# Kernel optimization log

Hardware: AMD Instinct MI355X
Metric: run time of the kernel (lower is better)

Reference implementation:

```python
import jax, jax.numpy as jnp
import numpy as np
from jax import lax

# Galaxy Zoo 2 question -> answer index ranges (start, end), keyed 1..11
Q_A = {1: (0, 3), 2: (3, 5), 3: (5, 7), 4: (7, 9), 5: (9, 13), 6: (13, 15),
       7: (15, 18), 8: (18, 25), 9: (25, 28), 10: (28, 31), 11: (31, 37)}
# Dependency map: answers whose probability multiplies the whole segment; [-1] = none
DEP = {1: [-1], 2: [1], 3: [4], 4: [4], 5: [4], 6: [-1],
       7: [0], 8: [13], 9: [3], 10: [7], 11: [7]}
BN_EPS = 1e-5


def _conv(x, w, b):
    y = lax.conv_general_dilated(x, w, (1, 1), 'VALID',
                                 dimension_numbers=('NCHW', 'OIHW', 'NCHW'))
    return y + b[None, :, None, None]


def _bn(x, s, b, m, v):  # eval-mode batchnorm with running stats
    inv = lax.rsqrt(v + BN_EPS)
    return (x - m[None, :, None, None]) * (s * inv)[None, :, None, None] + b[None, :, None, None]


def _pool(x):
    return lax.reduce_window(x, -jnp.inf, lax.max, (1, 1, 2, 2), (1, 1, 2, 2), 'VALID')


def _normalize(x):
    # Faithful to the in-place sequential torch loop: the segment sum is
    # recomputed after every element update, so earlier (already divided)
    # elements participate in later denominators. Fixed 37 steps, batched.
    for i in range(1, 12):
        s, e = Q_A[i]
        for j in range(s, e):
            seg_sum = jnp.sum(x[:, s:e], axis=1)
            x = x.at[:, j].set(x[:, j] / (seg_sum + 1e-12))
    return x


def _multiply_prob(x):
    # m = each[v] is read once before the inner j-loop, so a single
    # broadcast multiply over the segment is exactly equivalent.
    for i in range(1, 12):
        s, e = Q_A[i]
        vals = DEP[i]
        if vals[0] != -1:
            for v in vals:
                m = x[:, v:v + 1]  # [B,1], read before segment update
                x = x.at[:, s:e].multiply(m)
    return x


def _forward(x,
             conv1_w, conv1_b, bn1_s, bn1_b, bn1_m, bn1_v,
             conv2_w, conv2_b, bn2_s, bn2_b, bn2_m, bn2_v,
             conv3_w, conv3_b, bn3_s, bn3_b, bn3_m, bn3_v,
             conv4_w, conv4_b, bn4_s, bn4_b, bn4_m, bn4_v,
             fc1_w, fc1_b, fc2_w, fc2_b, fc3_w, fc3_b):
    # dropout layers are identity in eval mode
    h = _bn(jax.nn.relu(_conv(x, conv1_w, conv1_b)), bn1_s, bn1_b, bn1_m, bn1_v)
    h = _pool(_bn(jax.nn.relu(_conv(h, conv2_w, conv2_b)), bn2_s, bn2_b, bn2_m, bn2_v))
    h = _pool(_bn(jax.nn.relu(_conv(h, conv3_w, conv3_b)), bn3_s, bn3_b, bn3_m, bn3_v))
    h = _pool(_bn(jax.nn.relu(_conv(h, conv4_w, conv4_b)), bn4_s, bn4_b, bn4_m, bn4_v))
    h = h.reshape(-1, 3200)  # [B, 128*5*5]
    h = jax.nn.relu(h @ fc1_w.T + fc1_b)
    h = jax.nn.relu(h @ fc2_w.T + fc2_b)
    p = jax.nn.sigmoid(h @ fc3_w.T + fc3_b)  # [B, 37]
    return _multiply_prob(_normalize(p))


def setup_inputs() -> dict:
    key = jax.random.key(0)
    ks = iter(jax.random.split(key, 64))

    def n(shape, scale=0.05):
        return jax.random.normal(next(ks), shape, jnp.float32) * scale

    inp = {'x': jax.random.normal(next(ks), (1024, 3, 60, 60), jnp.float32)}
    convs = [(16, 3, 5), (32, 16, 5), (64, 32, 3), (128, 64, 3)]
    for ci, (o, i, kz) in enumerate(convs, 1):
        inp[f'conv{ci}_w'] = n((o, i, kz, kz))
        inp[f'conv{ci}_b'] = n((o,))
        inp[f'bn{ci}_s'] = 1.0 + n((o,))
        inp[f'bn{ci}_b'] = n((o,))
        inp[f'bn{ci}_m'] = n((o,))
        inp[f'bn{ci}_v'] = jax.random.uniform(next(ks), (o,), jnp.float32, 0.5, 1.5)
    inp['fc1_w'] = n((1024, 3200))
    inp['fc1_b'] = n((1024,))
    inp['fc2_w'] = n((512, 1024))
    inp['fc2_b'] = n((512,))
    inp['fc3_w'] = n((37, 512))
    inp['fc3_b'] = n((37,))
    return inp


def reference(x,
              conv1_w, conv1_b, bn1_s, bn1_b, bn1_m, bn1_v,
              conv2_w, conv2_b, bn2_s, bn2_b, bn2_m, bn2_v,
              conv3_w, conv3_b, bn3_s, bn3_b, bn3_m, bn3_v,
              conv4_w, conv4_b, bn4_s, bn4_b, bn4_m, bn4_v,
              fc1_w, fc1_b, fc2_w, fc2_b, fc3_w, fc3_b):
    return _forward(x,
                    conv1_w, conv1_b, bn1_s, bn1_b, bn1_m, bn1_v,
                    conv2_w, conv2_b, bn2_s, bn2_b, bn2_m, bn2_v,
                    conv3_w, conv3_b, bn3_s, bn3_b, bn3_m, bn3_v,
                    conv4_w, conv4_b, bn4_s, bn4_b, bn4_m, bn4_v,
                    fc1_w, fc1_b, fc2_w, fc2_b, fc3_w, fc3_b)
```

## Files before the change

kernel.cpp:

```cpp
#include <hip/hip_runtime.h>
#include <hip/hip_bf16.h>
#include <math.h>

constexpr int BATCH = 1024;
typedef unsigned short u16;
typedef unsigned long long u64;
typedef __attribute__((ext_vector_type(8))) short bf16x8;
typedef __attribute__((ext_vector_type(4))) float f32x4;
typedef __attribute__((ext_vector_type(16))) float f32x16;

__device__ __forceinline__ u16 f2bf(float f) {
    union { __hip_bfloat16 b; u16 s; } u; u.b = __float2bfloat16(f); return u.s;
}
__device__ __forceinline__ f32x4 mfma16(bf16x8 a, bf16x8 b, f32x4 c) {
    return __builtin_amdgcn_mfma_f32_16x16x32_bf16(a, b, c, 0, 0, 0);
}
__device__ __forceinline__ f32x16 mfma32(bf16x8 a, bf16x8 b, f32x16 c) {
    return __builtin_amdgcn_mfma_f32_32x32x16_bf16(a, b, c, 0, 0, 0);
}

__global__ __launch_bounds__(256)
void prep_all(const float* __restrict__ x,  const float* __restrict__ c1w,
              const float* __restrict__ c2w, const float* __restrict__ c3w,
              const float* __restrict__ c4w, const float* __restrict__ f1w,
              const float* __restrict__ f2w,
              u16* __restrict__ Xp,  u16* __restrict__ W1t, u16* __restrict__ W2t,
              u16* __restrict__ W3t, u16* __restrict__ W4t,
              u16* __restrict__ W1b, u16* __restrict__ W2b)
{
    int id = blockIdx.x * 256 + threadIdx.x;
    constexpr int NX   = 1024 * 3600;
    constexpr int NW1B = 819200;
    constexpr int NW2B = 131072;
    if (id < NX) {
        int img = id / 3600, p = id - img * 3600;
        const float* s = x + (size_t)img * 10800 + p;
        u16 pk[4] = { f2bf(s[0]), f2bf(s[3600]), f2bf(s[7200]), 0 };
        *(u64*)(Xp + (size_t)id * 4) = *(u64*)pk;
        return;
    }
    id -= NX;
    if (id < NW1B) {
        float4 v = ((const float4*)f1w)[id];
        u16 p[4] = { f2bf(v.x), f2bf(v.y), f2bf(v.z), f2bf(v.w) };
        *(u64*)(W1b + (size_t)id * 4) = *(u64*)p;
        return;
    }
    id -= NW1B;
    if (id < NW2B) {
        float4 v = ((const float4*)f2w)[id];
        u16 p[4] = { f2bf(v.x), f2bf(v.y), f2bf(v.z), f2bf(v.w) };
        *(u64*)(W2b + (size_t)id * 4) = *(u64*)p;
        return;
    }
    id -= NW2B;
    if (id < 2048) {
        int oc = id >> 7, k = id & 127, tap = k >> 2, ic = k & 3;
        W1t[id] = (ic < 3 && tap < 25) ? f2bf(c1w[oc * 75 + ic * 25 + tap]) : (u16)0;
        return;
    }
    id -= 2048;
    if (id < 12800) {
        int oc = id / 400, k = id - oc * 400;
        W2t[id] = f2bf(c2w[oc * 400 + (k & 15) * 25 + (k >> 4)]);
        return;
    }
    id -= 12800;
    if (id < 19456) {
        int oc = id / 304, k = id - oc * 304;
        W3t[id] = (k < 288) ? f2bf(c3w[oc * 288 + (k & 31) * 9 + (k >> 5)]) : (u16)0;
        return;
    }
    id -= 19456;
    if (id < 74752) {
        int oc = id / 584, k = id - oc * 584;
        W4t[id] = (k < 576) ? f2bf(c4w[oc * 576 + (k & 63) * 9 + (k >> 6)]) : (u16)0;
    }
}

__global__ __launch_bounds__(512, 4)
void conv12_fused(const u16* __restrict__ Xp,
                  const u16* __restrict__ W1t, const u16* __restrict__ W2t,
                  const float* __restrict__ c1b,
                  const float* __restrict__ b1s, const float* __restrict__ b1b,
                  const float* __restrict__ b1m, const float* __restrict__ b1v,
                  const float* __restrict__ c2b,
                  const float* __restrict__ b2s, const float* __restrict__ b2b,
                  const float* __restrict__ b2m, const float* __restrict__ b2v,
                  u16* __restrict__ out)
{
    __shared__ __align__(16) unsigned char S[54976];
    constexpr int U = 28800;
    float* s_bn1 = (float*)(S + 54400);
    float* s_bn2 = (float*)(S + 54592);

    const int tid = threadIdx.x;
    int bid = blockIdx.x;
    const int qx = bid & 1, qy = (bid >> 1) & 1, img = bid >> 2;

    const u64* XpI = (const u64*)Xp + (size_t)img * 3600 + (qy * 26) * 60 + qx * 26;
    for (int i = tid; i < 578; i += 512) {
        int row = i / 17, c2 = i - row * 17;
        *(bf16x8*)(S + U + (row * 34 + c2 * 2) * 8) =
            *(const bf16x8*)(XpI + row * 60 + c2 * 2);
    }
    for (int i = tid; i < 256; i += 512)
        *(bf16x8*)(S + U + 9248 + i * 16) = *(const bf16x8*)(W1t + i * 8);
    if (tid < 16) {
        float sc = b1s[tid] * rsqrtf(b1v[tid] + 1e-5f);
        s_bn1[tid] = c1b[tid]; s_bn1[16 + tid] = sc; s_bn1[32 + tid] = b1b[tid] - b1m[tid] * sc;
    } else if (tid >= 32 && tid < 64) {
        int t = tid - 32;
        float sc = b2s[t] * rsqrtf(b2v[t] + 1e-5f);
        s_bn2[t] = c2b[t]; s_bn2[32 + t] = sc; s_bn2[64 + t] = b2b[t] - b2m[t] * sc;
    }
    __syncthreads();

    const int wv = tid >> 6, lr = tid & 15, lg = (tid >> 4) & 3;
    const int o32 = tid & 31, hi = (tid >> 5) & 1;

    {
        int toff[4][2];
        #pragma unroll
        for (int ks = 0; ks < 4; ++ks)
            #pragma unroll
            for (int h = 0; h < 2; ++h) {
                int t = ks * 8 + lg * 2 + h; if (t > 24) t = 24;
                int ky = t / 5;
                toff[ks][h] = (ky * 34 + (t - ky * 5)) * 8;
            }
        bf16x8 wb[4];
        #pragma unroll
        for (int ks = 0; ks < 4; ++ks)
            wb[ks] = *(const bf16x8*)(S + U + 9248 + lr * 256 + ks * 64 + lg * 16);
        float4 bnB = *(const float4*)(s_bn1 + lg * 4);
        float4 bnS = *(const float4*)(s_bn1 + 16 + lg * 4);
        float4 bnH = *(const float4*)(s_bn1 + 32 + lg * 4);
        #pragma unroll
        for (int mi = 0; mi < 8; ++mi) {
            int t = wv + mi * 8;
            if (t < 57) {
                int pos = t * 16 + lr;
                int pc = pos > 899 ? 899 : pos;
                int py = pc / 30;
                int pb = (py * 34 + (pc - py * 30)) * 8;
                f32x4 a = {0.f, 0.f, 0.f, 0.f};
                #pragma unroll
                for (int ks = 0; ks < 4; ++ks) {
                    union { u64 v[2]; bf16x8 f; } xf;
                    xf.v[0] = *(const u64*)(S + U + pb + toff[ks][0]);
                    xf.v[1] = *(const u64*)(S + U + pb + toff[ks][1]);
                    a = mfma16(wb[ks], xf.f, a);
                }
                if (pos < 900) {
                    u16 q[4];
                    q[0] = f2bf(fmaxf(a[0] + bnB.x, 0.f) * bnS.x + bnH.x);
                    q[1] = f2bf(fmaxf(a[1] + bnB.y, 0.f) * bnS.y + bnH.y);
                    q[2] = f2bf(fmaxf(a[2] + bnB.z, 0.f) * bnS.z + bnH.z);
                    q[3] = f2bf(fmaxf(a[3] + bnB.w, 0.f) * bnS.w + bnH.w);
                    *(u64*)(S + pos * 32 + lg * 8) = *(u64*)q;
                }
            }
        }
    }
    __syncthreads();

    for (int i = tid; i < 1600; i += 512)
        *(bf16x8*)(S + U + i * 16) = *(const bf16x8*)(W2t + i * 8);
    __syncthreads();

    f32x16 acc[3];
    #pragma unroll
    for (int mi = 0; mi < 3; ++mi)
        #pragma unroll
        for (int j = 0; j < 16; ++j) acc[mi][j] = 0.f;
    int pbase[3];
    #pragma unroll
    for (int mi = 0; mi < 3; ++mi) {
        int tt = wv + mi * 8; if (tt > 21) tt = 21;
        int row = tt * 32 + o32;
        int q = row >> 2; if (q > 168) q = 168;
        int Q = row & 3;
        int y2 = 2 * (q / 13) + (Q >> 1);
        int x2 = 2 * (q - (q / 13) * 13) + (Q & 1);
        pbase[mi] = (y2 * 30 + x2) * 32 + hi * 16;
    }
    const unsigned char* wrow = S + U + o32 * 800 + hi * 16;
    #pragma unroll
    for (int ks = 0; ks < 25; ++ks) {
        bf16x8 b = *(const bf16x8*)(wrow + ks * 32);
        const int dp = ((ks / 5) * 30 + (ks % 5)) * 32;
        #pragma unroll
        for (int mi = 0; mi < 3; ++mi) {
            bf16x8 a = *(const bf16x8*)(S + pbase[mi] + dp);
            acc[mi] = mfma32(a, b, acc[mi]);
        }
    }
    u16* outI = out + (size_t)img * 676 * 32;
    float bnb = s_bn2[o32], bns = s_bn2[32 + o32], bnh = s_bn2[64 + o32];
    #pragma unroll
    for (int mi = 0; mi < 3; ++mi) {
        int tt = wv + mi * 8;
        if (tt < 22) {
            #pragma unroll
            for (int rg = 0; rg < 4; ++rg) {
                int quad = tt * 8 + 2 * rg + hi;
                if (quad < 169) {
                    float m = -3.4e38f;
                    #pragma unroll
                    for (int r = 0; r < 4; ++r)
                        m = fmaxf(m, fmaxf(acc[mi][rg * 4 + r] + bnb, 0.f) * bns + bnh);
                    int py = quad / 13, px = quad - (quad / 13) * 13;
                    int gpos = (qy * 13 + py) * 26 + qx * 13 + px;
                    outI[gpos * 32 + o32] = f2bf(m);
                }
            }
        }
    }
}

__global__ __launch_bounds__(576, 2)
void conv3_mfma(const u16* __restrict__ in, const u16* __restrict__ W3t,
                const float* __restrict__ cbias,
                const float* __restrict__ bns, const float* __restrict__ bnb,
                const float* __restrict__ bnm, const float* __restrict__ bnv,
                u16* __restrict__ out)
{
    __shared__ __align__(16) unsigned char S[63104];
    float* s_bn = (float*)(S + 62720);

    const int tid = threadIdx.x;
    const int ocg = blockIdx.x & 1;
    const int img = blockIdx.x >> 1;

    const u16* inI = in + (size_t)img * 676 * 32;
    for (int g = tid; g < 2704; g += 576) {
        int pa = g * 16;
        int off = pa ^ ((pa >> 2) & 0x20);
        *(bf16x8*)(S + off) = *(const bf16x8*)(inI + g * 8);
    }
    const u16* wsrc = W3t + ocg * 32 * 304;
    for (int i = tid; i < 1216; i += 576)
        *(bf16x8*)(S + 43264 + i * 16) = *(const bf16x8*)(wsrc + i * 8);
    if (tid < 32) {
        int oc = ocg * 32 + tid;
        float sc = bns[oc] * rsqrtf(bnv[oc] + 1e-5f);
        s_bn[tid] = cbias[oc]; s_bn[32 + tid] = sc; s_bn[64 + tid] = bnb[oc] - bnm[oc] * sc;
    }
    __syncthreads();

    const int wv = tid >> 6;
    const int o32 = tid & 31, hi = (tid >> 5) & 1;
    f32x16 acc[2];
    #pragma unroll
    for (int mi = 0; mi < 2; ++mi)
        #pragma unroll
        for (int j = 0; j < 16; ++j) acc[mi][j] = 0.f;
    int pbase[2];
    #pragma unroll
    for (int mi = 0; mi < 2; ++mi) {
        int tt = wv * 2 + mi;
        int row = tt * 32 + o32;
        int q = row >> 2, Q = row & 3;
        int y2 = 2 * (q / 12) + (Q >> 1);
        int x2 = 2 * (q - (q / 12) * 12) + (Q & 1);
        pbase[mi] = (y2 * 26 + x2) * 64 + hi * 16;
    }
    const unsigned char* wrow = S + 43264 + o32 * 608 + hi * 16;
    #pragma unroll
    for (int s = 0; s < 18; ++s) {
        bf16x8 b = *(const bf16x8*)(wrow + s * 32);
        const int cell = s >> 1;
        const int dp = ((cell / 3) * 26 + (cell % 3)) * 64 + (s & 1) * 32;
        #pragma unroll
        for (int mi = 0; mi < 2; ++mi) {
            int pa = pbase[mi] + dp;
            bf16x8 a = *(const bf16x8*)(S + (pa ^ ((pa >> 2) & 0x20)));
            acc[mi] = mfma32(a, b, acc[mi]);
        }
    }
    u16* outI = out + (size_t)img * 144 * 64 + ocg * 32;
    float bnbv = s_bn[o32], bnsv = s_bn[32 + o32], bnhv = s_bn[64 + o32];
    #pragma unroll
    for (int mi = 0; mi < 2; ++mi) {
        int tt = wv * 2 + mi;
        #pragma unroll
        for (int rg = 0; rg < 4; ++rg) {
            int quad = tt * 8 + 2 * rg + hi;
            float m = -3.4e38f;
            #pragma unroll
            for (int r = 0; r < 4; ++r)
                m = fmaxf(m, fmaxf(acc[mi][rg * 4 + r] + bnbv, 0.f) * bnsv + bnhv);
            outI[quad * 64 + o32] = f2bf(m);
        }
    }
}

__global__ __launch_bounds__(256)
void conv4_mfma(const u16* __restrict__ in, const u16* __restrict__ W4t,
                const float* __restrict__ cbias,
                const float* __restrict__ bns, const float* __restrict__ bnb,
                const float* __restrict__ bnm, const float* __restrict__ bnv,
                u16* __restrict__ out)
{
    __shared__ __align__(16) unsigned char S[56192];
    float* s_bn = (float*)(S + 55808);

    const int tid = threadIdx.x;
    const int ocg = blockIdx.x & 3;
    const int img = blockIdx.x >> 2;

    const u16* inI = in + (size_t)img * 144 * 64;
    for (int g = tid; g < 144 * 8; g += 256) {
        int pos = g >> 3, part = g & 7;
        int off = (pos * 128 + part * 16) ^ ((pos & 7) << 4);
        *(bf16x8*)(S + off) = *(const bf16x8*)(inI + g * 8);
    }
    const u16* wsrc = W4t + ocg * 32 * 584;
    for (int i = tid; i < 2336; i += 256)
        *(bf16x8*)(S + 18432 + i * 16) = *(const bf16x8*)(wsrc + i * 8);
    if (tid < 32) {
        int oc = ocg * 32 + tid;
        float sc = bns[oc] * rsqrtf(bnv[oc] + 1e-5f);
        s_bn[tid] = cbias[oc]; s_bn[32 + tid] = sc; s_bn[64 + tid] = bnb[oc] - bnm[oc] * sc;
    }
    __syncthreads();

    const int w = tid >> 6, lr = tid & 15, lg = (tid >> 4) & 3;
    f32x4 acc[2][2];
    {
        f32x4 z = {0.f, 0.f, 0.f, 0.f};
        acc[0][0] = z; acc[0][1] = z; acc[1][0] = z; acc[1][1] = z;
    }
    int pb7[2];
    #pragma unroll
    for (int mi = 0; mi < 2; ++mi) {
        int aq = (w + mi * 4) * 4 + (lr >> 2);
        if (aq > 24) aq = 24;
        int y2 = 2 * (aq / 5) + ((lr >> 1) & 1);
        int x2 = 2 * (aq % 5) + (lr & 1);
        pb7[mi] = ((y2 * 12 + x2) << 7) + lg * 16;
    }
    #pragma unroll
    for (int ks = 0; ks < 18; ++ks) {
        bf16x8 b0 = *(const bf16x8*)(S + 18432 + lr * 1168 + ks * 64 + lg * 16);
        bf16x8 b1 = *(const bf16x8*)(S + 18432 + (16 + lr) * 1168 + ks * 64 + lg * 16);
        const int cell = ks >> 1;
        const int dp7 = (((cell / 3) * 12 + (cell % 3)) << 7) + (ks & 1) * 64;
        #pragma unroll
        for (int mi = 0; mi < 2; ++mi) {
            int pa = pb7[mi] + dp7;
            int off = pa ^ ((pa >> 3) & 0x70);
            bf16x8 a = *(const bf16x8*)(S + off);
            acc[mi][0] = mfma16(a, b0, acc[mi][0]);
            acc[mi][1] = mfma16(a, b1, acc[mi][1]);
        }
    }
    u16* outI = out + (size_t)img * 3200;
    float bc0 = s_bn[lr],      sc0 = s_bn[32 + lr], sh0 = s_bn[64 + lr];
    float bc1 = s_bn[16 + lr], sc1 = s_bn[48 + lr], sh1 = s_bn[80 + lr];
    #pragma unroll
    for (int mi = 0; mi < 2; ++mi) {
        int quad = (w + mi * 4) * 4 + lg;
        if (quad < 25) {
            float m0 = -3.4e38f, m1 = -3.4e38f;
            #pragma unroll
            for (int r2 = 0; r2 < 4; ++r2) {
                m0 = fmaxf(m0, fmaxf(acc[mi][0][r2] + bc0, 0.f) * sc0 + sh0);
                m1 = fmaxf(m1, fmaxf(acc[mi][1][r2] + bc1, 0.f) * sc1 + sh1);
            }
            outI[(ocg * 32 + lr) * 25 + quad]      = f2bf(m0);
            outI[(ocg * 32 + 16 + lr) * 25 + quad] = f2bf(m1);
        }
    }
}

template<bool OUTF32>
__global__ __launch_bounds__(256)
void fc_gemm_bf(const u16* __restrict__ A, const u16* __restrict__ Wb,
                const float* __restrict__ bias, void* __restrict__ outv,
                int M, int N, int K)
{
    __shared__ __align__(16) unsigned char S[34816];
    const int tid = threadIdx.x;
    const int n0 = blockIdx.x * 64, m0 = blockIdx.y * 64;
    const int w = tid >> 6, lr = tid & 15, lg = (tid >> 4) & 3;
    const int r = tid >> 2, c = tid & 3;

    f32x4 acc[4];
    { f32x4 z = {0.f,0.f,0.f,0.f}; acc[0]=z; acc[1]=z; acc[2]=z; acc[3]=z; }

    const u16* Ab = A  + (size_t)(m0 + r) * K + c * 8;
    const u16* Bb = Wb + (size_t)(n0 + r) * K + c * 8;
    unsigned char* sAw = S + r * 272 + c * 16;
    unsigned char* sBw = S + 17408 + r * 272 + c * 16;

    for (int k0 = 0; k0 < K; k0 += 128) {
        #pragma unroll
        for (int q = 0; q < 4; ++q) {
            *(bf16x8*)(sAw + q * 64) = *(const bf16x8*)(Ab + k0 + q * 32);
            *(bf16x8*)(sBw + q * 64) = *(const bf16x8*)(Bb + k0 + q * 32);
        }
        __syncthreads();
        #pragma unroll
        for (int k32 = 0; k32 < 4; ++k32) {
            bf16x8 a = *(const bf16x8*)(S + (w * 16 + lr) * 272 + k32 * 64 + lg * 16);
            #pragma unroll
            for (int nt = 0; nt < 4; ++nt) {
                bf16x8 b = *(const bf16x8*)(S + 17408 + (nt * 16 + lr) * 272 + k32 * 64 + lg * 16);
                acc[nt] = mfma16(a, b, acc[nt]);
            }
        }
        __syncthreads();
    }
    #pragma unroll
    for (int nt = 0; nt < 4; ++nt) {
        int col = n0 + nt * 16 + lr;
        float bv = bias[col];
        #pragma unroll
        for (int r2 = 0; r2 < 4; ++r2) {
            int row = m0 + w * 16 + lg * 4 + r2;
            float v = fmaxf(acc[nt][r2] + bv, 0.f);
            if (OUTF32) ((float*)outv)[(size_t)row * N + col] = v;
            else        ((u16*)outv)[(size_t)row * N + col] = f2bf(v);
        }
    }
}

__global__ __launch_bounds__(256)
void fc3_norm(const float* __restrict__ A, const float* __restrict__ W,
              const float* __restrict__ bias, float* __restrict__ out)
{
    __shared__ float sp[4][40];
    const int v = threadIdx.x >> 6, lane = threadIdx.x & 63;
    const int img = blockIdx.x * 4 + v;

    if (lane < 37) {
        const float4* a4 = (const float4*)(A + (size_t)img * 512);
        const float4* w4 = (const float4*)(W + (size_t)lane * 512);
        float s = bias[lane];
        #pragma unroll 4
        for (int k = 0; k < 128; ++k) {
            float4 a = a4[k], ww = w4[k];
            s = fmaf(a.x, ww.x, s); s = fmaf(a.y, ww.y, s);
            s = fmaf(a.z, ww.z, s); s = fmaf(a.w, ww.w, s);
        }
        sp[v][lane] = 1.f / (1.f + expf(-s));
    }
    __syncthreads();
    if (lane == 0) {
        float xv[37];
        #pragma unroll
        for (int i = 0; i < 37; ++i) xv[i] = sp[v][i];
        const int ss[11]  = {0, 3, 5, 7, 9, 13, 15, 18, 25, 28, 31};
        const int ee[11]  = {3, 5, 7, 9, 13, 15, 18, 25, 28, 31, 37};
        const int dep[11] = {-1, 1, 4, 4, 4, -1, 0, 13, 3, 7, 7};
        #pragma unroll
        for (int i = 0; i < 11; ++i) {
            for (int j = ss[i]; j < ee[i]; ++j) {
                float ssum = 0.f;
                for (int cix = ss[i]; cix < ee[i]; ++cix) ssum += xv[cix];
                xv[j] = xv[j] / (ssum + 1e-12f);
            }
        }
        #pragma unroll
        for (int i = 0; i < 11; ++i) {
            if (dep[i] >= 0) {
                const float m = xv[dep[i]];
                for (int cix = ss[i]; cix < ee[i]; ++cix) xv[cix] *= m;
            }
        }
        #pragma unroll
        for (int i = 0; i < 37; ++i) sp[v][i] = xv[i];
    }
    __syncthreads();
    if (lane < 37) out[(size_t)img * 37 + lane] = sp[v][lane];
}

extern "C" void kernel_launch(void* const* d_in, const int* in_sizes, int n_in,
                              void* d_out, int out_size, void* d_ws, size_t ws_size,
                              hipStream_t stream)
{
    const float* x   = (const float*)d_in[0];
    const float* c1w = (const float*)d_in[1];  const float* c1b = (const float*)d_in[2];
    const float* b1s = (const float*)d_in[3];  const float* b1b = (const float*)d_in[4];
    const float* b1m = (const float*)d_in[5];  const float* b1v = (const float*)d_in[6];
    const float* c2w = (const float*)d_in[7];  const float* c2b = (const float*)d_in[8];
    const float* b2s = (const float*)d_in[9];  const float* b2b = (const float*)d_in[10];
    const float* b2m = (const float*)d_in[11]; const float* b2v = (const float*)d_in[12];
    const float* c3w = (const float*)d_in[13]; const float* c3b = (const float*)d_in[14];
    const float* b3s = (const float*)d_in[15]; const float* b3b = (const float*)d_in[16];
    const float* b3m = (const float*)d_in[17]; const float* b3v = (const float*)d_in[18];
    const float* c4w = (const float*)d_in[19]; const float* c4b = (const float*)d_in[20];
    const float* b4s = (const float*)d_in[21]; const float* b4b = (const float*)d_in[22];
    const float* b4m = (const float*)d_in[23]; const float* b4v = (const float*)d_in[24];
    const float* f1w = (const float*)d_in[25]; const float* f1b = (const float*)d_in[26];
    const float* f2w = (const float*)d_in[27]; const float* f2b = (const float*)d_in[28];
    const float* f3w = (const float*)d_in[29]; const float* f3b = (const float*)d_in[30];

    u16*   P2  = (u16*)d_ws;
    u16*   Xp  = (u16*)((char*)d_ws + 44302336);
    u16*   P3  = (u16*)((char*)d_ws + 44302336);
    u16*   P4  = (u16*)((char*)d_ws + 63176704);
    u16*   F1  = (u16*)((char*)d_ws + 69730304);
    float* F2  = (float*)((char*)d_ws + 71827456);
    u16*   W1b = (u16*)((char*)d_ws + 73924608);
    u16*   W2b = (u16*)((char*)d_ws + 80478208);
    u16*   W1t = (u16*)((char*)d_ws + 81526784);
    u16*   W2t = (u16*)((char*)d_ws + 81530880);
    u16*   W3t = (u16*)((char*)d_ws + 81556480);
    u16*   W4t = (u16*)((char*)d_ws + 81595392);

    prep_all<<<4745728 / 256, 256, 0, stream>>>(x, c1w, c2w, c3w, c4w, f1w, f2w,
                                                Xp, W1t, W2t, W3t, W4t, W1b, W2b);

    conv12_fused<<<BATCH * 4, 512, 0, stream>>>(Xp, W1t, W2t, c1b, b1s, b1b, b1m, b1v,
                                                c2b, b2s, b2b, b2m, b2v, P2);
    conv3_mfma<<<BATCH * 2, 576, 0, stream>>>(P2, W3t, c3b, b3s, b3b, b3m, b3v, P3);
    conv4_mfma<<<BATCH * 4, 256, 0, stream>>>(P3, W4t, c4b, b4s, b4b, b4m, b4v, P4);

    fc_gemm_bf<false><<<dim3(16, 16), 256, 0, stream>>>(P4, W1b, f1b, F1, 1024, 1024, 3200);
    fc_gemm_bf<true ><<<dim3(8, 16),  256, 0, stream>>>(F1, W2b, f2b, F2, 1024, 512, 1024);
    fc3_norm<<<BATCH / 4, 256, 0, stream>>>(F2, f3w, f3b, (float*)d_out);
}
```

Measured before the change: 268.5 us.

## Read conv weights from global in MFMA fragment order instead of staging in LDS

The prep kernel now writes conv2/3/4 weights pre-permuted into the exact per-lane MFMA B-fragment order. Each conv kernel then loads those fragments straight from global memory (expected to hit L2) rather than copying them into shared memory first. This drops the LDS weight staging loops and one barrier, and shrinks the LDS footprint, and the launch bounds are raised to allow more resident blocks. The cost is per-iteration global-memory latency inside the MFMA loops and tighter register limits from the higher occupancy targets.

```diff
diff --git a/kernel.cpp b/kernel.cpp
--- a/kernel.cpp
+++ b/kernel.cpp
@@ -24,8 +24,8 @@
               const float* __restrict__ c2w, const float* __restrict__ c3w,
               const float* __restrict__ c4w, const float* __restrict__ f1w,
               const float* __restrict__ f2w,
-              u16* __restrict__ Xp,  u16* __restrict__ W1t, u16* __restrict__ W2t,
-              u16* __restrict__ W3t, u16* __restrict__ W4t,
+              u16* __restrict__ Xp,  u16* __restrict__ W1t, u16* __restrict__ W2g,
+              u16* __restrict__ W3g, u16* __restrict__ W4g,
               u16* __restrict__ W1b, u16* __restrict__ W2b)
 {
     int id = blockIdx.x * 256 + threadIdx.x;
@@ -61,26 +61,37 @@
     }
     id -= 2048;
     if (id < 12800) {
-        int oc = id / 400, k = id - oc * 400;
-        W2t[id] = f2bf(c2w[oc * 400 + (k & 15) * 25 + (k >> 4)]);
+        int ks = id / 512, r = id & 511;
+        int o32 = r >> 4, hi = (r >> 3) & 1, j = r & 7;
+        int k = ks * 16 + hi * 8 + j;
+        W2g[id] = f2bf(c2w[o32 * 400 + (k & 15) * 25 + (k >> 4)]);
         return;
     }
     id -= 12800;
-    if (id < 19456) {
-        int oc = id / 304, k = id - oc * 304;
-        W3t[id] = (k < 288) ? f2bf(c3w[oc * 288 + (k & 31) * 9 + (k >> 5)]) : (u16)0;
+    if (id < 18432) {
+        int ocg = id / 9216, r = id % 9216;
+        int s = r / 512, r2 = r & 511;
+        int o32 = r2 >> 4, hi = (r2 >> 3) & 1, j = r2 & 7;
+        int k = s * 16 + hi * 8 + j;
+        W3g[id] = f2bf(c3w[(ocg * 32 + o32) * 288 + (k & 31) * 9 + (k >> 5)]);
         return;
     }
-    id -= 19456;
-    if (id < 74752) {
-        int oc = id / 584, k = id - oc * 584;
-        W4t[id] = (k < 576) ? f2bf(c4w[oc * 576 + (k & 63) * 9 + (k >> 6)]) : (u16)0;
-    }
-}
-
-__global__ __launch_bounds__(512, 4)
+    id -= 18432;
+    if (id < 73728) {
+        int ocg = id / 18432, r = id % 18432;
+        int ks = r / 1024, r2 = r & 1023;
+        int half = r2 >> 9, r3 = r2 & 511;
+        int lr = r3 >> 5, r4 = r3 & 31;
+        int lg = r4 >> 3, j = r4 & 7;
+        int k = ks * 32 + lg * 8 + j;
+        int oc = ocg * 32 + half * 16 + lr;
+        W4g[id] = f2bf(c4w[oc * 576 + (k & 63) * 9 + (k >> 6)]);
+    }
+}
+
+__global__ __launch_bounds__(512, 6)
 void conv12_fused(const u16* __restrict__ Xp,
-                  const u16* __restrict__ W1t, const u16* __restrict__ W2t,
+                  const u16* __restrict__ W1t, const u16* __restrict__ W2g,
                   const float* __restrict__ c1b,
                   const float* __restrict__ b1s, const float* __restrict__ b1b,
                   const float* __restrict__ b1m, const float* __restrict__ b1v,
@@ -89,10 +100,9 @@
                   const float* __restrict__ b2m, const float* __restrict__ b2v,
                   u16* __restrict__ out)
 {
-    __shared__ __align__(16) unsigned char S[54976];
-    constexpr int U = 28800;
-    float* s_bn1 = (float*)(S + 54400);
-    float* s_bn2 = (float*)(S + 54592);
+    __shared__ __align__(16) unsigned char S[42720];
+    float* s_bn1 = (float*)(S + 42144);
+    float* s_bn2 = (float*)(S + 42336);
 
     const int tid = threadIdx.x;
     int bid = blockIdx.x;
@@ -101,11 +111,11 @@
     const u64* XpI = (const u64*)Xp + (size_t)img * 3600 + (qy * 26) * 60 + qx * 26;
     for (int i = tid; i < 578; i += 512) {
         int row = i / 17, c2 = i - row * 17;
-        *(bf16x8*)(S + U + (row * 34 + c2 * 2) * 8) =
+        *(bf16x8*)(S + 28800 + (row * 34 + c2 * 2) * 8) =
             *(const bf16x8*)(XpI + row * 60 + c2 * 2);
     }
     for (int i = tid; i < 256; i += 512)
-        *(bf16x8*)(S + U + 9248 + i * 16) = *(const bf16x8*)(W1t + i * 8);
+        *(bf16x8*)(S + 38048 + i * 16) = *(const bf16x8*)(W1t + i * 8);
     if (tid < 16) {
         float sc = b1s[tid] * rsqrtf(b1v[tid] + 1e-5f);
         s_bn1[tid] = c1b[tid]; s_bn1[16 + tid] = sc; s_bn1[32 + tid] = b1b[tid] - b1m[tid] * sc;
@@ -132,7 +142,7 @@
         bf16x8 wb[4];
         #pragma unroll
         for (int ks = 0; ks < 4; ++ks)
-            wb[ks] = *(const bf16x8*)(S + U + 9248 + lr * 256 + ks * 64 + lg * 16);
+            wb[ks] = *(const bf16x8*)(S + 38048 + lr * 256 + ks * 64 + lg * 16);
         float4 bnB = *(const float4*)(s_bn1 + lg * 4);
         float4 bnS = *(const float4*)(s_bn1 + 16 + lg * 4);
         float4 bnH = *(const float4*)(s_bn1 + 32 + lg * 4);
@@ -148,8 +158,8 @@
                 #pragma unroll
                 for (int ks = 0; ks < 4; ++ks) {
                     union { u64 v[2]; bf16x8 f; } xf;
-                    xf.v[0] = *(const u64*)(S + U + pb + toff[ks][0]);
-                    xf.v[1] = *(const u64*)(S + U + pb + toff[ks][1]);
+                    xf.v[0] = *(const u64*)(S + 28800 + pb + toff[ks][0]);
+                    xf.v[1] = *(const u64*)(S + 28800 + pb + toff[ks][1]);
                     a = mfma16(wb[ks], xf.f, a);
                 }
                 if (pos < 900) {
@@ -165,10 +175,6 @@
     }
     __syncthreads();
 
-    for (int i = tid; i < 1600; i += 512)
-        *(bf16x8*)(S + U + i * 16) = *(const bf16x8*)(W2t + i * 8);
-    __syncthreads();
-
     f32x16 acc[3];
     #pragma unroll
     for (int mi = 0; mi < 3; ++mi)
@@ -185,10 +191,11 @@
         int x2 = 2 * (q - (q / 13) * 13) + (Q & 1);
         pbase[mi] = (y2 * 30 + x2) * 32 + hi * 16;
     }
-    const unsigned char* wrow = S + U + o32 * 800 + hi * 16;
+    const bf16x8* W2v = (const bf16x8*)W2g;
+    const int bidx = o32 * 2 + hi;
     #pragma unroll
     for (int ks = 0; ks < 25; ++ks) {
-        bf16x8 b = *(const bf16x8*)(wrow + ks * 32);
+        bf16x8 b = W2v[ks * 64 + bidx];
         const int dp = ((ks / 5) * 30 + (ks % 5)) * 32;
         #pragma unroll
         for (int mi = 0; mi < 3; ++mi) {
@@ -219,15 +226,15 @@
     }
 }
 
-__global__ __launch_bounds__(576, 2)
-void conv3_mfma(const u16* __restrict__ in, const u16* __restrict__ W3t,
+__global__ __launch_bounds__(576, 6)
+void conv3_mfma(const u16* __restrict__ in, const u16* __restrict__ W3g,
                 const float* __restrict__ cbias,
                 const float* __restrict__ bns, const float* __restrict__ bnb,
                 const float* __restrict__ bnm, const float* __restrict__ bnv,
                 u16* __restrict__ out)
 {
-    __shared__ __align__(16) unsigned char S[63104];
-    float* s_bn = (float*)(S + 62720);
+    __shared__ __align__(16) unsigned char S[43648];
+    float* s_bn = (float*)(S + 43264);
 
     const int tid = threadIdx.x;
     const int ocg = blockIdx.x & 1;
@@ -239,9 +246,6 @@
         int off = pa ^ ((pa >> 2) & 0x20);
         *(bf16x8*)(S + off) = *(const bf16x8*)(inI + g * 8);
     }
-    const u16* wsrc = W3t + ocg * 32 * 304;
-    for (int i = tid; i < 1216; i += 576)
-        *(bf16x8*)(S + 43264 + i * 16) = *(const bf16x8*)(wsrc + i * 8);
     if (tid < 32) {
         int oc = ocg * 32 + tid;
         float sc = bns[oc] * rsqrtf(bnv[oc] + 1e-5f);
@@ -266,10 +270,11 @@
         int x2 = 2 * (q - (q / 12) * 12) + (Q & 1);
         pbase[mi] = (y2 * 26 + x2) * 64 + hi * 16;
     }
-    const unsigned char* wrow = S + 43264 + o32 * 608 + hi * 16;
+    const bf16x8* W3v = (const bf16x8*)W3g;
+    const int bidx = ocg * 1152 + o32 * 2 + hi;
     #pragma unroll
     for (int s = 0; s < 18; ++s) {
-        bf16x8 b = *(const bf16x8*)(wrow + s * 32);
+        bf16x8 b = W3v[bidx + s * 64];
         const int cell = s >> 1;
         const int dp = ((cell / 3) * 26 + (cell % 3)) * 64 + (s & 1) * 32;
         #pragma unroll
@@ -296,15 +301,15 @@
     }
 }
 
-__global__ __launch_bounds__(256)
-void conv4_mfma(const u16* __restrict__ in, const u16* __restrict__ W4t,
+__global__ __launch_bounds__(256, 8)
+void conv4_mfma(const u16* __restrict__ in, const u16* __restrict__ W4g,
                 const float* __restrict__ cbias,
                 const float* __restrict__ bns, const float* __restrict__ bnb,
                 const float* __restrict__ bnm, const float* __restrict__ bnv,
                 u16* __restrict__ out)
 {
-    __shared__ __align__(16) unsigned char S[56192];
-    float* s_bn = (float*)(S + 55808);
+    __shared__ __align__(16) unsigned char S[18816];
+    float* s_bn = (float*)(S + 18432);
 
     const int tid = threadIdx.x;
     const int ocg = blockIdx.x & 3;
@@ -316,9 +321,6 @@
         int off = (pos * 128 + part * 16) ^ ((pos & 7) << 4);
         *(bf16x8*)(S + off) = *(const bf16x8*)(inI + g * 8);
     }
-    const u16* wsrc = W4t + ocg * 32 * 584;
-    for (int i = tid; i < 2336; i += 256)
-        *(bf16x8*)(S + 18432 + i * 16) = *(const bf16x8*)(wsrc + i * 8);
     if (tid < 32) {
         int oc = ocg * 32 + tid;
         float sc = bns[oc] * rsqrtf(bnv[oc] + 1e-5f);
@@ -341,10 +343,12 @@
         int x2 = 2 * (aq % 5) + (lr & 1);
         pb7[mi] = ((y2 * 12 + x2) << 7) + lg * 16;
     }
+    const bf16x8* W4v = (const bf16x8*)W4g;
+    const int base = ocg * 2304 + lr * 4 + lg;
     #pragma unroll
     for (int ks = 0; ks < 18; ++ks) {
-        bf16x8 b0 = *(const bf16x8*)(S + 18432 + lr * 1168 + ks * 64 + lg * 16);
-        bf16x8 b1 = *(const bf16x8*)(S + 18432 + (16 + lr) * 1168 + ks * 64 + lg * 16);
+        bf16x8 b0 = W4v[base + ks * 128];
+        bf16x8 b1 = W4v[base + ks * 128 + 64];
         const int cell = ks >> 1;
         const int dp7 = (((cell / 3) * 12 + (cell % 3)) << 7) + (ks & 1) * 64;
         #pragma unroll
@@ -507,17 +511,17 @@
     u16*   W1b = (u16*)((char*)d_ws + 73924608);
     u16*   W2b = (u16*)((char*)d_ws + 80478208);
     u16*   W1t = (u16*)((char*)d_ws + 81526784);
-    u16*   W2t = (u16*)((char*)d_ws + 81530880);
-    u16*   W3t = (u16*)((char*)d_ws + 81556480);
-    u16*   W4t = (u16*)((char*)d_ws + 81595392);
-
-    prep_all<<<4745728 / 256, 256, 0, stream>>>(x, c1w, c2w, c3w, c4w, f1w, f2w,
-                                                Xp, W1t, W2t, W3t, W4t, W1b, W2b);
-
-    conv12_fused<<<BATCH * 4, 512, 0, stream>>>(Xp, W1t, W2t, c1b, b1s, b1b, b1m, b1v,
+    u16*   W2g = (u16*)((char*)d_ws + 81530880);
+    u16*   W3g = (u16*)((char*)d_ws + 81556480);
+    u16*   W4g = (u16*)((char*)d_ws + 81593344);
+
+    prep_all<<<18530, 256, 0, stream>>>(x, c1w, c2w, c3w, c4w, f1w, f2w,
+                                        Xp, W1t, W2g, W3g, W4g, W1b, W2b);
+
+    conv12_fused<<<BATCH * 4, 512, 0, stream>>>(Xp, W1t, W2g, c1b, b1s, b1b, b1m, b1v,
                                                 c2b, b2s, b2b, b2m, b2v, P2);
-    conv3_mfma<<<BATCH * 2, 576, 0, stream>>>(P2, W3t, c3b, b3s, b3b, b3m, b3v, P3);
-    conv4_mfma<<<BATCH * 4, 256, 0, stream>>>(P3, W4t, c4b, b4s, b4b, b4m, b4v, P4);
+    conv3_mfma<<<BATCH * 2, 576, 0, stream>>>(P2, W3g, c3b, b3s, b3b, b3m, b3v, P3);
+    conv4_mfma<<<BATCH * 4, 256, 0, stream>>>(P3, W4g, c4b, b4s, b4b, b4m, b4v, P4);
 
     fc_gemm_bf<false><<<dim3(16, 16), 256, 0, stream>>>(P4, W1b, f1b, F1, 1024, 1024, 3200);
     fc_gemm_bf<true ><<<dim3(8, 16),  256, 0, stream>>>(F1, W2b, f2b, F2, 1024, 512, 1024);
```

Result: faster. 245.8 us (-8.5%).
